# Kernel tuning notes

Measured on AMD Instinct MI355X. Metric: run time of the kernel, lower is better.

## Reference

```python
import jax, jax.numpy as jnp
import numpy as np

B, T, DIN, P, HID, L = 256, 512, 25, 128, 256, 5
Q = 0.15
EPS = 1e-5


def setup_inputs() -> dict:
    key = jax.random.key(0)
    ks = jax.random.split(key, 12)
    s = 0.05
    return {
        "x": jax.random.normal(ks[0], (B, T, DIN), jnp.float32),
        "lengths": jax.random.randint(ks[1], (B,), 1, T + 1),
        "ln_g": jnp.ones((DIN,), jnp.float32),
        "ln_b": jnp.zeros((DIN,), jnp.float32),
        "w1": jax.random.normal(ks[2], (DIN, P), jnp.float32) * s,
        "b1": jnp.zeros((P,), jnp.float32),
        "w2": jax.random.normal(ks[3], (P, P), jnp.float32) * s,
        "b2": jnp.zeros((P,), jnp.float32),
        "Wih0": jax.random.normal(ks[4], (2, 3 * HID, P), jnp.float32) * s,
        "Whh0": jax.random.normal(ks[5], (2, 3 * HID, HID), jnp.float32) * s,
        "bih0": jnp.zeros((2, 3 * HID), jnp.float32),
        "bhh0": jnp.zeros((2, 3 * HID), jnp.float32),
        "Wih": jax.random.normal(ks[6], (L - 1, 2, 3 * HID, 2 * HID), jnp.float32) * s,
        "Whh": jax.random.normal(ks[7], (L - 1, 2, 3 * HID, HID), jnp.float32) * s,
        "bih": jnp.zeros((L - 1, 2, 3 * HID), jnp.float32),
        "bhh": jnp.zeros((L - 1, 2, 3 * HID), jnp.float32),
        "Wc": jax.random.normal(ks[8], (2 * HID,), jnp.float32) * s,
        "bc": jnp.zeros((), jnp.float32),
    }


def _gru_dir(xs, mask, Wih, Whh, bih, bhh):
    """Masked unidirectional GRU (PyTorch gate convention). xs:[B,T,Din], mask:[B,T] -> [B,T,HID]."""
    xw = jnp.einsum('btd,gd->btg', xs, Wih) + bih  # [B,T,3H] precomputed input gates

    def step(h, inp):
        xw_t, m_t = inp  # [B,3H], [B]
        gh = h @ Whh.T + bhh
        r = jax.nn.sigmoid(xw_t[:, :HID] + gh[:, :HID])
        z = jax.nn.sigmoid(xw_t[:, HID:2 * HID] + gh[:, HID:2 * HID])
        n = jnp.tanh(xw_t[:, 2 * HID:] + r * gh[:, 2 * HID:])
        h_new = (1.0 - z) * n + z * h
        h = jnp.where(m_t[:, None], h_new, h)        # hold state past sequence end (packing)
        return h, jnp.where(m_t[:, None], h, 0.0)    # padded outputs are zero (pad_packed)

    h0 = jnp.zeros((xs.shape[0], HID), xs.dtype)
    _, ys = jax.lax.scan(step, h0, (xw.transpose(1, 0, 2), mask.T))
    return ys.transpose(1, 0, 2)


def reference(x, lengths, ln_g, ln_b, w1, b1, w2, b2,
              Wih0, Whh0, bih0, bhh0, Wih, Whh, bih, bhh, Wc, bc):
    mask = jnp.arange(T)[None, :] < lengths[:, None]  # [B,T]

    # InputProjection: LayerNorm -> Linear -> GELU(exact) -> Linear
    mu = x.mean(-1, keepdims=True)
    var = ((x - mu) ** 2).mean(-1, keepdims=True)
    xn = (x - mu) / jnp.sqrt(var + EPS) * ln_g + ln_b
    h = jax.nn.gelu(xn @ w1 + b1, approximate=False) @ w2 + b2  # [B,T,P]

    # per-sample time reversal indices (reverse valid prefix only)
    rev = jnp.clip(lengths[:, None] - 1 - jnp.arange(T)[None, :], 0, T - 1)  # [B,T]

    inp = h
    for l in range(L):
        Wi = Wih0 if l == 0 else Wih[l - 1]
        Wh = Whh0 if l == 0 else Whh[l - 1]
        bi = bih0 if l == 0 else bih[l - 1]
        bh = bhh0 if l == 0 else bhh[l - 1]
        yf = _gru_dir(inp, mask, Wi[0], Wh[0], bi[0], bh[0])
        x_rev = jnp.take_along_axis(inp, rev[:, :, None], axis=1) * mask[:, :, None]
        yb_rev = _gru_dir(x_rev, mask, Wi[1], Wh[1], bi[1], bh[1])
        yb = jnp.take_along_axis(yb_rev, rev[:, :, None], axis=1) * mask[:, :, None]
        inp = jnp.concatenate([yf, yb], axis=-1)  # [B,T,2H]
    H = inp

    # TopQPooling: per-sample variable-k top-k by L2-norm score, then mean
    scores = jnp.where(mask, jnp.linalg.norm(H, axis=2), -1e9)
    k_vals = jnp.maximum(jnp.ceil(lengths.astype(jnp.float32) * Q).astype(jnp.int32), 1)  # [B]
    order = jnp.argsort(-scores, axis=1)                      # descending by score
    topmask = jnp.arange(T)[None, :] < k_vals[:, None]        # first k of sorted order
    Hs = jnp.take_along_axis(H, order[:, :, None], axis=1)
    pooled = (Hs * topmask[:, :, None]).sum(axis=1) / k_vals[:, None].astype(H.dtype)

    logits = pooled @ Wc + bc  # [B]
    return logits
```

## Files before the change

### kernel.cpp

```cpp
#include <hip/hip_runtime.h>
#include <math.h>


#define CH 64

#define AT_LOAD_RLX(p)    __hip_atomic_load((p),  __ATOMIC_RELAXED, __HIP_MEMORY_SCOPE_AGENT)
#define AT_LOAD_ACQ(p)    __hip_atomic_load((p),  __ATOMIC_ACQUIRE, __HIP_MEMORY_SCOPE_AGENT)
#define AT_STORE_RLX(p,v) __hip_atomic_store((p),(v),__ATOMIC_RELAXED, __HIP_MEMORY_SCOPE_AGENT)
#define AT_STORE_REL(p,v) __hip_atomic_store((p),(v),__ATOMIC_RELEASE, __HIP_MEMORY_SCOPE_AGENT)

__global__ __launch_bounds__(256)
void sort_k(const int* __restrict__ len, int* __restrict__ perm,
            int* __restrict__ nchp, int Bg)
{
    __shared__ int ll[256];
    __shared__ int lp[256];
    const int i = threadIdx.x;
    const int li = len[i];
    ll[i] = li;
    __syncthreads();
    int rk = 0;
    for (int j = 0; j < 256; j++) {
        int lj = ll[j];
        rk += (lj < li || (lj == li && j < i)) ? 1 : 0;
    }
    lp[rk] = i;
    __syncthreads();
    perm[i] = lp[i];
    const int ngrp = 256 / Bg;
    if (i < ngrp) {
        int mx = ll[lp[i * Bg + Bg - 1]];
        int nch = (mx + 63) >> 6;
        nchp[i] = nch < 1 ? 1 : (nch > 8 ? 8 : nch);
    }
}

__global__ __launch_bounds__(256)
void prep_whhT_k(const float* __restrict__ Whh0, const float* __restrict__ Whh,
                 float* __restrict__ out)
{
    int id = blockIdx.x * 256 + threadIdx.x;
    int k  = id & 31;
    int q  = id >> 5;
    int g  = q % 3;  q /= 3;
    int t  = q & 255; q >>= 8;
    int sl = q & 7;   q >>= 3;
    int l  = q >> 1, d = q & 1;
    int row = g * 256 + sl * 32 + (t & 31);
    int col = (t >> 5) * 32 + k;
    out[id] = (l == 0) ? Whh0[(size_t)(d * 768 + row) * 256 + col]
                       : Whh[(size_t)(((l - 1) * 2 + d) * 768 + row) * 256 + col];
}

__global__ __launch_bounds__(128)
void input_proj_k(const float* __restrict__ x, const int* __restrict__ lengths,
                  const int* __restrict__ perm,
                  const float* __restrict__ lng, const float* __restrict__ lnb,
                  const float* __restrict__ w1, const float* __restrict__ b1v,
                  const float* __restrict__ w2, const float* __restrict__ b2v,
                  float* __restrict__ out, int g0)
{
    const int btl = blockIdx.x;
    const int sl  = btl >> 9;
    const int t   = btl & 511;
    const int b   = perm[g0 + sl];
    if (t >= lengths[b]) return;
    const int tid = threadIdx.x;
    __shared__ float xs[25];
    __shared__ float xn[25];
    __shared__ float hs[128];
    if (tid < 25) xs[tid] = x[((size_t)b * 512 + t) * 25 + tid];
    __syncthreads();
    if (tid < 25) {
        float mu = 0.f;
        #pragma unroll
        for (int k = 0; k < 25; k++) mu += xs[k];
        mu *= (1.f / 25.f);
        float var = 0.f;
        #pragma unroll
        for (int k = 0; k < 25; k++) { float dd = xs[k] - mu; var += dd * dd; }
        var *= (1.f / 25.f);
        float rstd = 1.f / sqrtf(var + 1e-5f);
        xn[tid] = (xs[tid] - mu) * rstd * lng[tid] + lnb[tid];
    }
    __syncthreads();
    float a = b1v[tid];
    #pragma unroll
    for (int k = 0; k < 25; k++) a = fmaf(xn[k], w1[k * 128 + tid], a);
    float ge = 0.5f * a * (1.f + erff(a * 0.70710678118654752440f));
    hs[tid] = ge;
    __syncthreads();
    float o = b2v[tid];
    #pragma unroll 8
    for (int k = 0; k < 128; k++) o = fmaf(hs[k], w2[k * 128 + tid], o);
    out[(size_t)btl * 128 + tid] = o;
}

__global__ __launch_bounds__(256, 1)
void round_k(const float* __restrict__ A, int K,
             const float* __restrict__ W,
             const float* __restrict__ bi,
             const int* __restrict__ lengths, const int* __restrict__ perm,
             const int* __restrict__ nchp, int gidx, int g0, int Bg,
             float* __restrict__ xw_w,
             const float* __restrict__ xw_r,
             const float* __restrict__ whhT,
             const float* __restrict__ bhh,
             float* __restrict__ Y,
             int* __restrict__ hx,
             int* __restrict__ flags,
             int NR, int r, int epoch)
{
    __shared__ float smem[8192];

    const int tid = threadIdx.x;
    const int nch = nchp[gidx];

    if ((int)blockIdx.x < NR) {
        if (r == 0) return;
        const int sgN = Bg >> 3;
        const int S2  = 2 * sgN;
        const int q   = (int)blockIdx.x % S2;
        const int sl  = (int)blockIdx.x / S2;
        const int d   = (q >= sgN) ? 1 : 0;
        const int sg  = q - d * sgN;
        const int lo  = d ? (nch - r) * CH : (r - 1) * CH;
        if (lo < 0 || lo >= 512) return;
        const int mlsg = lengths[perm[g0 + sg * 8 + 7]];
        int nst = min(lo + CH, mlsg) - lo;
        if (nst <= 0) return;
        const bool first = d ? (mlsg <= lo + CH) : (r == 1);

        float* hf   = smem;
        float* gsbp = smem + 2048;

        const int kq = tid >> 5;
        const int jj = tid & 31;

        const float* wb = whhT + ((size_t)(d * 8 + sl) * 256 + tid) * 96;
        float w0[32], w1[32], w2[32];
        #pragma unroll
        for (int k4 = 0; k4 < 8; k4++) {
            float4 a = *(const float4*)(wb + k4 * 4);
            float4 b = *(const float4*)(wb + 32 + k4 * 4);
            float4 c = *(const float4*)(wb + 64 + k4 * 4);
            w0[k4 * 4 + 0] = a.x; w0[k4 * 4 + 1] = a.y;
            w0[k4 * 4 + 2] = a.z; w0[k4 * 4 + 3] = a.w;
            w1[k4 * 4 + 0] = b.x; w1[k4 * 4 + 1] = b.y;
            w1[k4 * 4 + 2] = b.z; w1[k4 * 4 + 3] = b.w;
            w2[k4 * 4 + 0] = c.x; w2[k4 * 4 + 1] = c.y;
            w2[k4 * 4 + 2] = c.z; w2[k4 * 4 + 3] = c.w;
        }
        #pragma unroll
        for (int k = 0; k < 32; k++)
            asm volatile("" : "+v"(w0[k]), "+v"(w1[k]), "+v"(w2[k]));

        const int s2 = tid >> 5;
        const int j2 = tid & 31;
        const int lens2 = lengths[perm[g0 + sg * 8 + s2]];
        const float bh0 = bhh[d * 768 +       sl * 32 + j2];
        const float bh1 = bhh[d * 768 + 256 + sl * 32 + j2];
        const float bh2 = bhh[d * 768 + 512 + sl * 32 + j2];
        int* flg = flags + (size_t)((d * sgN + sg) * 8) * 64;
        const int PS  = 2 * Bg * 256;
        const int hxq = (d * Bg + sg * 8) * 256;

        if (first) {
            #pragma unroll
            for (int i = 0; i < 8; i++) hf[i * 256 + tid] = 0.f;
        } else {
            const int pprev = d ? (lo + nst) : (lo - 1);
            const int par0  = pprev & 1;
            const int* src = hx + par0 * PS + hxq;
            #pragma unroll
            for (int i = 0; i < 8; i++)
                hf[i * 256 + tid] = __int_as_float(AT_LOAD_RLX(src + i * 256 + tid));
        }
        __syncthreads();

        const float* xwd = xw_r + (size_t)(d * Bg + sg * 8) * 64 * 768 + sl * 32 + j2;

        for (int st = 0; st < nst; st++) {
            const int p   = d ? (lo + nst - 1 - st) : (lo + st);
            const int row = p - lo;
            const float* xr = xwd + (size_t)(s2 * 64 + row) * 768;
            const float xv0 = xr[0], xv1 = xr[256], xv2 = xr[512];

            #pragma unroll
            for (int s = 0; s < 8; s++) {
                float b0 = 0.f, b1 = 0.f, b2 = 0.f;
                #pragma unroll
                for (int k4 = 0; k4 < 8; k4++) {
                    const float4 h4 = *(const float4*)&hf[s * 256 + kq * 32 + k4 * 4];
                    b0 = fmaf(h4.x, w0[k4 * 4 + 0], b0);
                    b0 = fmaf(h4.y, w0[k4 * 4 + 1], b0);
                    b0 = fmaf(h4.z, w0[k4 * 4 + 2], b0);
                    b0 = fmaf(h4.w, w0[k4 * 4 + 3], b0);
                    b1 = fmaf(h4.x, w1[k4 * 4 + 0], b1);
                    b1 = fmaf(h4.y, w1[k4 * 4 + 1], b1);
                    b1 = fmaf(h4.z, w1[k4 * 4 + 2], b1);
                    b1 = fmaf(h4.w, w1[k4 * 4 + 3], b1);
                    b2 = fmaf(h4.x, w2[k4 * 4 + 0], b2);
                    b2 = fmaf(h4.y, w2[k4 * 4 + 1], b2);
                    b2 = fmaf(h4.z, w2[k4 * 4 + 2], b2);
                    b2 = fmaf(h4.w, w2[k4 * 4 + 3], b2);
                }
                gsbp[(kq * 8 + s) * 96 + jj]      = b0;
                gsbp[(kq * 8 + s) * 96 + 32 + jj] = b1;
                gsbp[(kq * 8 + s) * 96 + 64 + jj] = b2;
            }
            __syncthreads();

            float gr = bh0, gz = bh1, gn = bh2;
            #pragma unroll
            for (int qq = 0; qq < 8; qq++) {
                gr += gsbp[(qq * 8 + s2) * 96 + j2];
                gz += gsbp[(qq * 8 + s2) * 96 + 32 + j2];
                gn += gsbp[(qq * 8 + s2) * 96 + 64 + j2];
            }
            const float rg = 1.f / (1.f + expf(-(xv0 + gr)));
            const float zg = 1.f / (1.f + expf(-(xv1 + gz)));
            const float ng = tanhf(xv2 + rg * gn);
            const float hv = hf[s2 * 256 + sl * 32 + j2];
            float hn = (1.f - zg) * ng + zg * hv;
            if (p >= lens2) hn = hv;
            const int par = p & 1;
            AT_STORE_RLX(&hx[par * PS + hxq + s2 * 256 + sl * 32 + j2],
                         __float_as_int(hn));
            if (p < lens2)
                Y[((size_t)((sg * 8 + s2) * 512 + p)) * 512 + d * 256 + sl * 32 + j2] = hn;
            __syncthreads();

            if (st == nst - 1) break;
            if (tid == 0) AT_STORE_REL(&flg[sl * 64 + st], epoch);
            if (tid < 8) {
                int* f = &flg[tid * 64 + st];
                while (AT_LOAD_ACQ(f) != epoch) __builtin_amdgcn_s_sleep(2);
            }
            __syncthreads();
            {
                const int* src = hx + par * PS + hxq;
                #pragma unroll
                for (int i = 0; i < 8; i++)
                    hf[i * 256 + tid] = __int_as_float(
                        AT_LOAD_RLX(src + i * 256 + tid));
            }
            __syncthreads();
        }
    } else {
        float (*As)[68]  = (float(*)[68])smem;
        float (*Bs)[132] = (float(*)[132])(smem + 544);

        const int gid  = blockIdx.x - NR;
        const int nt   = gid % 6;
        const int rest = gid / 6;
        const int d    = (rest >= Bg) ? 1 : 0;
        const int s    = rest - d * Bg;
        const int lo   = d ? (nch - 1 - r) * 64 : r * 64;
        if (lo < 0 || lo >= 512) return;
        if (lengths[perm[g0 + s]] <= lo) return;

        float acc[4][8] = {};
        const int tm = tid >> 4;
        const int tn = tid & 15;
        const int arr = tid >> 2, ak = (tid & 3) * 2;
        const int bn = tid >> 1, bk = (tid & 1) * 4;

        const float* Ap = A + (size_t)(s * 512 + lo + arr) * K + ak;
        const float* Wp = W + ((size_t)d * 768 + nt * 128 + bn) * K + bk;

        for (int k0 = 0; k0 < K; k0 += 8) {
            float2 av = *(const float2*)(Ap + k0);
            float4 bv = *(const float4*)(Wp + k0);
            __syncthreads();
            As[ak][arr] = av.x; As[ak + 1][arr] = av.y;
            Bs[bk + 0][bn] = bv.x; Bs[bk + 1][bn] = bv.y;
            Bs[bk + 2][bn] = bv.z; Bs[bk + 3][bn] = bv.w;
            __syncthreads();
            #pragma unroll
            for (int kk = 0; kk < 8; kk++) {
                float4 a4 = *(const float4*)&As[kk][tm * 4];
                float4 b0v = *(const float4*)&Bs[kk][tn * 4];
                float4 b1v = *(const float4*)&Bs[kk][64 + tn * 4];
                float ar4[4] = {a4.x, a4.y, a4.z, a4.w};
                float br[8] = {b0v.x, b0v.y, b0v.z, b0v.w,
                               b1v.x, b1v.y, b1v.z, b1v.w};
                #pragma unroll
                for (int i = 0; i < 4; i++)
                    #pragma unroll
                    for (int j = 0; j < 8; j++)
                        acc[i][j] = fmaf(ar4[i], br[j], acc[i][j]);
            }
        }
        const int cb = d * 768 + nt * 128;
        float bv0[4], bv1[4];
        #pragma unroll
        for (int j = 0; j < 4; j++) {
            bv0[j] = bi[cb + tn * 4 + j];
            bv1[j] = bi[cb + 64 + tn * 4 + j];
        }
        #pragma unroll
        for (int i = 0; i < 4; i++) {
            const int row = tm * 4 + i;
            float* o = xw_w + (size_t)((d * Bg + s) * 64 + row) * 768 + nt * 128 + tn * 4;
            float4 c0 = make_float4(acc[i][0] + bv0[0], acc[i][1] + bv0[1],
                                    acc[i][2] + bv0[2], acc[i][3] + bv0[3]);
            float4 c1 = make_float4(acc[i][4] + bv1[0], acc[i][5] + bv1[1],
                                    acc[i][6] + bv1[2], acc[i][7] + bv1[3]);
            *(float4*)(o)      = c0;
            *(float4*)(o + 64) = c1;
        }
    }
}

__global__ __launch_bounds__(256)
void pool_k(const float* __restrict__ H, const int* __restrict__ lengths,
            const int* __restrict__ perm,
            const float* __restrict__ Wc, const float* __restrict__ bcp,
            float* __restrict__ out, int g0)
{
    const int bl = blockIdx.x;
    const int b  = perm[g0 + bl];
    const int tid = threadIdx.x;
    __shared__ float sc[512];
    __shared__ int   sel[128];
    __shared__ int   nsel;
    __shared__ float red[256];
    const int len = lengths[b];
    const int k = max(1, (int)ceilf((float)len * 0.15f));
    if (tid == 0) nsel = 0;
    for (int t = tid; t < 512; t += 256) {
        float s;
        if (t < len) {
            const float* row = H + ((size_t)bl * 512 + t) * 512;
            float acc = 0.f;
            for (int j = 0; j < 512; j++) acc = fmaf(row[j], row[j], acc);
            s = sqrtf(acc);
        } else s = -1e9f;
        sc[t] = s;
    }
    __syncthreads();
    for (int t = tid; t < 512; t += 256) {
        if (t < len) {
            const float s = sc[t];
            int cnt = 0;
            for (int u = 0; u < 512; u++) {
                float su = sc[u];
                cnt += (su > s || (su == s && u < t)) ? 1 : 0;
            }
            if (cnt < k) { int p = atomicAdd(&nsel, 1); sel[p] = t; }
        }
    }
    __syncthreads();
    const int ns = nsel;
    float part = 0.f;
    for (int j = tid; j < 512; j += 256) {
        float acc = 0.f;
        for (int i = 0; i < ns; i++)
            acc += H[((size_t)bl * 512 + sel[i]) * 512 + j];
        part += (acc / (float)k) * Wc[j];
    }
    red[tid] = part;
    __syncthreads();
    for (int s2 = 128; s2 > 0; s2 >>= 1) {
        if (tid < s2) red[tid] += red[tid + s2];
        __syncthreads();
    }
    if (tid == 0) out[b] = red[0] + bcp[0];
}

static inline size_t alup(size_t x) { return (x + 255) & ~255ull; }

static size_t tier_bytes(int Bg)
{
    return 2 * alup((size_t)Bg * 512 * 512 * 4)
         + 2 * alup((size_t)Bg * 2 * 64 * 768 * 4)
         + alup(1966080ull * 4)
         + alup((size_t)4 * Bg * 256 * 4)
         + alup((size_t)2 * (Bg / 8) * 8 * 64 * 4)
         + alup(2048);
}

extern "C" void kernel_launch(void* const* d_in, const int* in_sizes, int n_in,
                              void* d_out, int out_size, void* d_ws, size_t ws_size,
                              hipStream_t stream)
{
    const float* x    = (const float*)d_in[0];
    const int*   len  = (const int*)  d_in[1];
    const float* ln_g = (const float*)d_in[2];
    const float* ln_b = (const float*)d_in[3];
    const float* w1   = (const float*)d_in[4];
    const float* b1   = (const float*)d_in[5];
    const float* w2   = (const float*)d_in[6];
    const float* b2   = (const float*)d_in[7];
    const float* Wih0 = (const float*)d_in[8];
    const float* Whh0 = (const float*)d_in[9];
    const float* bih0 = (const float*)d_in[10];
    const float* bhh0 = (const float*)d_in[11];
    const float* Wih  = (const float*)d_in[12];
    const float* Whh  = (const float*)d_in[13];
    const float* bih  = (const float*)d_in[14];
    const float* bhh  = (const float*)d_in[15];
    const float* Wc   = (const float*)d_in[16];
    const float* bc   = (const float*)d_in[17];
    float* out = (float*)d_out;

    int Bg = 0;
    const int tiers[5] = {128, 64, 32, 16, 8};
    for (int i = 0; i < 5; i++)
        if (ws_size >= tier_bytes(tiers[i])) { Bg = tiers[i]; break; }
    if (Bg == 0) return;

    char* ws = (char*)d_ws;
    size_t off = 0;
    auto alloc = [&](size_t bytes) { size_t o = off; off += alup(bytes); return o; };
    float* h0    = (float*)(ws + alloc((size_t)Bg * 512 * 512 * 4));
    float* h1    = (float*)(ws + alloc((size_t)Bg * 512 * 512 * 4));
    float* xwA   = (float*)(ws + alloc((size_t)Bg * 2 * 64 * 768 * 4));
    float* xwB   = (float*)(ws + alloc((size_t)Bg * 2 * 64 * 768 * 4));
    float* whhT  = (float*)(ws + alloc(1966080ull * 4));
    int*   hx    = (int*)  (ws + alloc((size_t)4 * Bg * 256 * 4));
    const size_t flagBytes = (size_t)2 * (Bg / 8) * 8 * 64 * 4;
    int*   flags = (int*)  (ws + alloc(flagBytes));
    int*   perm  = (int*)  (ws + alloc(2048));
    int*   nchp  = perm + 256;
    float* xwbuf[2] = {xwA, xwB};

    hipMemsetAsync(flags, 0, flagBytes, stream);

    sort_k<<<1, 256, 0, stream>>>(len, perm, nchp, Bg);
    prep_whhT_k<<<7680, 256, 0, stream>>>(Whh0, Whh, whhT);

    const int NR = 2 * Bg;
    const int NG = 12 * Bg;

    for (int g0 = 0; g0 < 256; g0 += Bg) {
        const int gidx = g0 / Bg;
        input_proj_k<<<Bg * 512, 128, 0, stream>>>(x, len, perm, ln_g, ln_b,
                                                   w1, b1, w2, b2, h0, g0);
        float* bin = h0;
        float* bout = h1;
        for (int l = 0; l < 5; l++) {
            const int K = (l == 0) ? 128 : 512;
            const float* Wl  = (l == 0) ? Wih0 : (Wih + (size_t)(l - 1) * 2 * 768 * 512);
            const float* bil = (l == 0) ? bih0 : (bih + (size_t)(l - 1) * 1536);
            const float* whl = whhT + (size_t)l * 393216;
            const float* bhl = (l == 0) ? bhh0 : (bhh + (size_t)(l - 1) * 1536);
            for (int r = 0; r <= 8; r++) {
                const int ep = (gidx * 5 + l) * 9 + r + 1;
                round_k<<<NR + NG, 256, 0, stream>>>(
                    bin, K, Wl, bil, len, perm, nchp, gidx, g0, Bg,
                    xwbuf[r & 1], xwbuf[(r & 1) ^ 1],
                    whl, bhl, bout, hx, flags, NR, r, ep);
            }
            float* tmp = bin; bin = bout; bout = tmp;
        }
        pool_k<<<Bg, 256, 0, stream>>>(bin, len, perm, Wc, bc, out, g0);
    }
}
```

Measured before the change: 56.23 ms.

## Split fused round kernel into separate GEMM and recurrence launches, weights in LDS

Replaces the single launch that mixed input-projection GEMM blocks with recurrence blocks by two separate launches per round: gemm_k, then recur_k. The recurrence kernel now stages its recurrent weight slice in swizzled LDS instead of holding 96 floats per thread in registers, which frees VGPRs. In exchange the GEMM for the next chunk no longer overlaps with the current recurrence, there are more kernel launches, and each step adds LDS reads for the weights.

```diff
diff --git a/kernel.cpp b/kernel.cpp
--- a/kernel.cpp
+++ b/kernel.cpp
@@ -97,219 +97,220 @@
 }
 
 __global__ __launch_bounds__(256, 1)
-void round_k(const float* __restrict__ A, int K,
-             const float* __restrict__ W,
-             const float* __restrict__ bi,
-             const int* __restrict__ lengths, const int* __restrict__ perm,
+void recur_k(const int* __restrict__ lengths, const int* __restrict__ perm,
              const int* __restrict__ nchp, int gidx, int g0, int Bg,
-             float* __restrict__ xw_w,
              const float* __restrict__ xw_r,
              const float* __restrict__ whhT,
              const float* __restrict__ bhh,
              float* __restrict__ Y,
              int* __restrict__ hx,
              int* __restrict__ flags,
-             int NR, int r, int epoch)
-{
-    __shared__ float smem[8192];
+             int r, int epoch)
+{
+    __shared__ float wlds[24576];
+    __shared__ float hf[2048];
+    __shared__ float gsbp[6144];
 
     const int tid = threadIdx.x;
     const int nch = nchp[gidx];
-
-    if ((int)blockIdx.x < NR) {
-        if (r == 0) return;
-        const int sgN = Bg >> 3;
-        const int S2  = 2 * sgN;
-        const int q   = (int)blockIdx.x % S2;
-        const int sl  = (int)blockIdx.x / S2;
-        const int d   = (q >= sgN) ? 1 : 0;
-        const int sg  = q - d * sgN;
-        const int lo  = d ? (nch - r) * CH : (r - 1) * CH;
-        if (lo < 0 || lo >= 512) return;
-        const int mlsg = lengths[perm[g0 + sg * 8 + 7]];
-        int nst = min(lo + CH, mlsg) - lo;
-        if (nst <= 0) return;
-        const bool first = d ? (mlsg <= lo + CH) : (r == 1);
-
-        float* hf   = smem;
-        float* gsbp = smem + 2048;
-
-        const int kq = tid >> 5;
-        const int jj = tid & 31;
-
-        const float* wb = whhT + ((size_t)(d * 8 + sl) * 256 + tid) * 96;
-        float w0[32], w1[32], w2[32];
+    const int sgN = Bg >> 3;
+    const int S2  = 2 * sgN;
+    const int q   = (int)blockIdx.x % S2;
+    const int sl  = (int)blockIdx.x / S2;
+    const int d   = (q >= sgN) ? 1 : 0;
+    const int sg  = q - d * sgN;
+    const int lo  = d ? (nch - r) * CH : (r - 1) * CH;
+    if (lo < 0 || lo >= 512) return;
+    const int mlsg = lengths[perm[g0 + sg * 8 + 7]];
+    int nst = min(lo + CH, mlsg) - lo;
+    if (nst <= 0) return;
+    const bool first = d ? (mlsg <= lo + CH) : (r == 1);
+
+    const float* wb = whhT + ((size_t)(d * 8 + sl) * 256 + tid) * 96;
+    float* wt = wlds + tid * 96;
+    const int cx = tid & 7;
+    #pragma unroll
+    for (int i = 0; i < 24; i++) {
+        const float4 v = *(const float4*)(wb + i * 4);
+        *(float4*)(wt + ((i ^ cx) << 2)) = v;
+    }
+
+    const int kq = tid >> 5;
+    const int jj = tid & 31;
+    const int s2 = tid >> 5;
+    const int j2 = tid & 31;
+    const int lens2 = lengths[perm[g0 + sg * 8 + s2]];
+    const float bh0 = bhh[d * 768 +       sl * 32 + j2];
+    const float bh1 = bhh[d * 768 + 256 + sl * 32 + j2];
+    const float bh2 = bhh[d * 768 + 512 + sl * 32 + j2];
+    int* flg = flags + (size_t)((d * sgN + sg) * 8) * 64;
+    const int PS  = 2 * Bg * 256;
+    const int hxq = (d * Bg + sg * 8) * 256;
+
+    if (first) {
+        #pragma unroll
+        for (int i = 0; i < 8; i++) hf[i * 256 + tid] = 0.f;
+    } else {
+        const int pprev = d ? (lo + nst) : (lo - 1);
+        const int par0  = pprev & 1;
+        const int* src = hx + par0 * PS + hxq;
+        #pragma unroll
+        for (int i = 0; i < 8; i++)
+            hf[i * 256 + tid] = __int_as_float(AT_LOAD_RLX(src + i * 256 + tid));
+    }
+    __syncthreads();
+
+    const float* xwd = xw_r + (size_t)(d * Bg + sg * 8) * 64 * 768 + sl * 32 + j2;
+
+    for (int st = 0; st < nst; st++) {
+        const int p   = d ? (lo + nst - 1 - st) : (lo + st);
+        const int row = p - lo;
+        const float* xr = xwd + (size_t)(s2 * 64 + row) * 768;
+        const float xv0 = xr[0], xv1 = xr[256], xv2 = xr[512];
+
+        float a0[8], a1[8], a2[8];
+        #pragma unroll
+        for (int s = 0; s < 8; s++) { a0[s] = 0.f; a1[s] = 0.f; a2[s] = 0.f; }
         #pragma unroll
         for (int k4 = 0; k4 < 8; k4++) {
-            float4 a = *(const float4*)(wb + k4 * 4);
-            float4 b = *(const float4*)(wb + 32 + k4 * 4);
-            float4 c = *(const float4*)(wb + 64 + k4 * 4);
-            w0[k4 * 4 + 0] = a.x; w0[k4 * 4 + 1] = a.y;
-            w0[k4 * 4 + 2] = a.z; w0[k4 * 4 + 3] = a.w;
-            w1[k4 * 4 + 0] = b.x; w1[k4 * 4 + 1] = b.y;
-            w1[k4 * 4 + 2] = b.z; w1[k4 * 4 + 3] = b.w;
-            w2[k4 * 4 + 0] = c.x; w2[k4 * 4 + 1] = c.y;
-            w2[k4 * 4 + 2] = c.z; w2[k4 * 4 + 3] = c.w;
-        }
-        #pragma unroll
-        for (int k = 0; k < 32; k++)
-            asm volatile("" : "+v"(w0[k]), "+v"(w1[k]), "+v"(w2[k]));
-
-        const int s2 = tid >> 5;
-        const int j2 = tid & 31;
-        const int lens2 = lengths[perm[g0 + sg * 8 + s2]];
-        const float bh0 = bhh[d * 768 +       sl * 32 + j2];
-        const float bh1 = bhh[d * 768 + 256 + sl * 32 + j2];
-        const float bh2 = bhh[d * 768 + 512 + sl * 32 + j2];
-        int* flg = flags + (size_t)((d * sgN + sg) * 8) * 64;
-        const int PS  = 2 * Bg * 256;
-        const int hxq = (d * Bg + sg * 8) * 256;
-
-        if (first) {
+            const int sw = (k4 ^ cx) << 2;
+            const float4 w0 = *(const float4*)(wt + sw);
+            const float4 w1 = *(const float4*)(wt + 32 + sw);
+            const float4 w2 = *(const float4*)(wt + 64 + sw);
             #pragma unroll
-            for (int i = 0; i < 8; i++) hf[i * 256 + tid] = 0.f;
-        } else {
-            const int pprev = d ? (lo + nst) : (lo - 1);
-            const int par0  = pprev & 1;
-            const int* src = hx + par0 * PS + hxq;
+            for (int s = 0; s < 8; s++) {
+                const float4 h4 = *(const float4*)&hf[s * 256 + kq * 32 + k4 * 4];
+                a0[s] = fmaf(h4.x, w0.x, a0[s]);
+                a0[s] = fmaf(h4.y, w0.y, a0[s]);
+                a0[s] = fmaf(h4.z, w0.z, a0[s]);
+                a0[s] = fmaf(h4.w, w0.w, a0[s]);
+                a1[s] = fmaf(h4.x, w1.x, a1[s]);
+                a1[s] = fmaf(h4.y, w1.y, a1[s]);
+                a1[s] = fmaf(h4.z, w1.z, a1[s]);
+                a1[s] = fmaf(h4.w, w1.w, a1[s]);
+                a2[s] = fmaf(h4.x, w2.x, a2[s]);
+                a2[s] = fmaf(h4.y, w2.y, a2[s]);
+                a2[s] = fmaf(h4.z, w2.z, a2[s]);
+                a2[s] = fmaf(h4.w, w2.w, a2[s]);
+            }
+        }
+        #pragma unroll
+        for (int s = 0; s < 8; s++) {
+            gsbp[(kq * 8 + s) * 96 + jj]      = a0[s];
+            gsbp[(kq * 8 + s) * 96 + 32 + jj] = a1[s];
+            gsbp[(kq * 8 + s) * 96 + 64 + jj] = a2[s];
+        }
+        __syncthreads();
+
+        float gr = bh0, gz = bh1, gn = bh2;
+        #pragma unroll
+        for (int qq = 0; qq < 8; qq++) {
+            gr += gsbp[(qq * 8 + s2) * 96 + j2];
+            gz += gsbp[(qq * 8 + s2) * 96 + 32 + j2];
+            gn += gsbp[(qq * 8 + s2) * 96 + 64 + j2];
+        }
+        const float rg = 1.f / (1.f + expf(-(xv0 + gr)));
+        const float zg = 1.f / (1.f + expf(-(xv1 + gz)));
+        const float ng = tanhf(xv2 + rg * gn);
+        const float hv = hf[s2 * 256 + sl * 32 + j2];
+        float hn = (1.f - zg) * ng + zg * hv;
+        if (p >= lens2) hn = hv;
+        const int par = p & 1;
+        AT_STORE_RLX(&hx[par * PS + hxq + s2 * 256 + sl * 32 + j2],
+                     __float_as_int(hn));
+        if (p < lens2)
+            Y[((size_t)((sg * 8 + s2) * 512 + p)) * 512 + d * 256 + sl * 32 + j2] = hn;
+        __syncthreads();
+
+        if (st == nst - 1) break;
+        if (tid == 0) AT_STORE_REL(&flg[sl * 64 + st], epoch);
+        if (tid < 8) {
+            int* f = &flg[tid * 64 + st];
+            while (AT_LOAD_ACQ(f) != epoch) __builtin_amdgcn_s_sleep(2);
+        }
+        __syncthreads();
+        {
+            const int* src = hx + par * PS + hxq;
             #pragma unroll
             for (int i = 0; i < 8; i++)
-                hf[i * 256 + tid] = __int_as_float(AT_LOAD_RLX(src + i * 256 + tid));
-        }
-        __syncthreads();
-
-        const float* xwd = xw_r + (size_t)(d * Bg + sg * 8) * 64 * 768 + sl * 32 + j2;
-
-        for (int st = 0; st < nst; st++) {
-            const int p   = d ? (lo + nst - 1 - st) : (lo + st);
-            const int row = p - lo;
-            const float* xr = xwd + (size_t)(s2 * 64 + row) * 768;
-            const float xv0 = xr[0], xv1 = xr[256], xv2 = xr[512];
-
+                hf[i * 256 + tid] = __int_as_float(
+                    AT_LOAD_RLX(src + i * 256 + tid));
+        }
+        __syncthreads();
+    }
+}
+
+__global__ __launch_bounds__(256)
+void gemm_k(const float* __restrict__ A, int K,
+            const float* __restrict__ W,
+            const float* __restrict__ bi,
+            const int* __restrict__ lengths, const int* __restrict__ perm,
+            const int* __restrict__ nchp, int gidx, int g0, int Bg,
+            float* __restrict__ xw_w, int r)
+{
+    __shared__ float As[8][68];
+    __shared__ float Bs[8][132];
+
+    const int tid = threadIdx.x;
+    const int nch = nchp[gidx];
+    const int gid  = blockIdx.x;
+    const int nt   = gid % 6;
+    const int rest = gid / 6;
+    const int d    = (rest >= Bg) ? 1 : 0;
+    const int s    = rest - d * Bg;
+    const int lo   = d ? (nch - 1 - r) * 64 : r * 64;
+    if (lo < 0 || lo >= 512) return;
+    if (lengths[perm[g0 + s]] <= lo) return;
+
+    float acc[4][8] = {};
+    const int tm = tid >> 4;
+    const int tn = tid & 15;
+    const int arr = tid >> 2, ak = (tid & 3) * 2;
+    const int bn = tid >> 1, bk = (tid & 1) * 4;
+
+    const float* Ap = A + (size_t)(s * 512 + lo + arr) * K + ak;
+    const float* Wp = W + ((size_t)d * 768 + nt * 128 + bn) * K + bk;
+
+    for (int k0 = 0; k0 < K; k0 += 8) {
+        float2 av = *(const float2*)(Ap + k0);
+        float4 bv = *(const float4*)(Wp + k0);
+        __syncthreads();
+        As[ak][arr] = av.x; As[ak + 1][arr] = av.y;
+        Bs[bk + 0][bn] = bv.x; Bs[bk + 1][bn] = bv.y;
+        Bs[bk + 2][bn] = bv.z; Bs[bk + 3][bn] = bv.w;
+        __syncthreads();
+        #pragma unroll
+        for (int kk = 0; kk < 8; kk++) {
+            float4 a4 = *(const float4*)&As[kk][tm * 4];
+            float4 b0v = *(const float4*)&Bs[kk][tn * 4];
+            float4 b1v = *(const float4*)&Bs[kk][64 + tn * 4];
+            float ar4[4] = {a4.x, a4.y, a4.z, a4.w};
+            float br[8] = {b0v.x, b0v.y, b0v.z, b0v.w,
+                           b1v.x, b1v.y, b1v.z, b1v.w};
             #pragma unroll
-            for (int s = 0; s < 8; s++) {
-                float b0 = 0.f, b1 = 0.f, b2 = 0.f;
+            for (int i = 0; i < 4; i++)
                 #pragma unroll
-                for (int k4 = 0; k4 < 8; k4++) {
-                    const float4 h4 = *(const float4*)&hf[s * 256 + kq * 32 + k4 * 4];
-                    b0 = fmaf(h4.x, w0[k4 * 4 + 0], b0);
-                    b0 = fmaf(h4.y, w0[k4 * 4 + 1], b0);
-                    b0 = fmaf(h4.z, w0[k4 * 4 + 2], b0);
-                    b0 = fmaf(h4.w, w0[k4 * 4 + 3], b0);
-                    b1 = fmaf(h4.x, w1[k4 * 4 + 0], b1);
-                    b1 = fmaf(h4.y, w1[k4 * 4 + 1], b1);
-                    b1 = fmaf(h4.z, w1[k4 * 4 + 2], b1);
-                    b1 = fmaf(h4.w, w1[k4 * 4 + 3], b1);
-                    b2 = fmaf(h4.x, w2[k4 * 4 + 0], b2);
-                    b2 = fmaf(h4.y, w2[k4 * 4 + 1], b2);
-                    b2 = fmaf(h4.z, w2[k4 * 4 + 2], b2);
-                    b2 = fmaf(h4.w, w2[k4 * 4 + 3], b2);
-                }
-                gsbp[(kq * 8 + s) * 96 + jj]      = b0;
-                gsbp[(kq * 8 + s) * 96 + 32 + jj] = b1;
-                gsbp[(kq * 8 + s) * 96 + 64 + jj] = b2;
-            }
-            __syncthreads();
-
-            float gr = bh0, gz = bh1, gn = bh2;
-            #pragma unroll
-            for (int qq = 0; qq < 8; qq++) {
-                gr += gsbp[(qq * 8 + s2) * 96 + j2];
-                gz += gsbp[(qq * 8 + s2) * 96 + 32 + j2];
-                gn += gsbp[(qq * 8 + s2) * 96 + 64 + j2];
-            }
-            const float rg = 1.f / (1.f + expf(-(xv0 + gr)));
-            const float zg = 1.f / (1.f + expf(-(xv1 + gz)));
-            const float ng = tanhf(xv2 + rg * gn);
-            const float hv = hf[s2 * 256 + sl * 32 + j2];
-            float hn = (1.f - zg) * ng + zg * hv;
-            if (p >= lens2) hn = hv;
-            const int par = p & 1;
-            AT_STORE_RLX(&hx[par * PS + hxq + s2 * 256 + sl * 32 + j2],
-                         __float_as_int(hn));
-            if (p < lens2)
-                Y[((size_t)((sg * 8 + s2) * 512 + p)) * 512 + d * 256 + sl * 32 + j2] = hn;
-            __syncthreads();
-
-            if (st == nst - 1) break;
-            if (tid == 0) AT_STORE_REL(&flg[sl * 64 + st], epoch);
-            if (tid < 8) {
-                int* f = &flg[tid * 64 + st];
-                while (AT_LOAD_ACQ(f) != epoch) __builtin_amdgcn_s_sleep(2);
-            }
-            __syncthreads();
-            {
-                const int* src = hx + par * PS + hxq;
-                #pragma unroll
-                for (int i = 0; i < 8; i++)
-                    hf[i * 256 + tid] = __int_as_float(
-                        AT_LOAD_RLX(src + i * 256 + tid));
-            }
-            __syncthreads();
-        }
-    } else {
-        float (*As)[68]  = (float(*)[68])smem;
-        float (*Bs)[132] = (float(*)[132])(smem + 544);
-
-        const int gid  = blockIdx.x - NR;
-        const int nt   = gid % 6;
-        const int rest = gid / 6;
-        const int d    = (rest >= Bg) ? 1 : 0;
-        const int s    = rest - d * Bg;
-        const int lo   = d ? (nch - 1 - r) * 64 : r * 64;
-        if (lo < 0 || lo >= 512) return;
-        if (lengths[perm[g0 + s]] <= lo) return;
-
-        float acc[4][8] = {};
-        const int tm = tid >> 4;
-        const int tn = tid & 15;
-        const int arr = tid >> 2, ak = (tid & 3) * 2;
-        const int bn = tid >> 1, bk = (tid & 1) * 4;
-
-        const float* Ap = A + (size_t)(s * 512 + lo + arr) * K + ak;
-        const float* Wp = W + ((size_t)d * 768 + nt * 128 + bn) * K + bk;
-
-        for (int k0 = 0; k0 < K; k0 += 8) {
-            float2 av = *(const float2*)(Ap + k0);
-            float4 bv = *(const float4*)(Wp + k0);
-            __syncthreads();
-            As[ak][arr] = av.x; As[ak + 1][arr] = av.y;
-            Bs[bk + 0][bn] = bv.x; Bs[bk + 1][bn] = bv.y;
-            Bs[bk + 2][bn] = bv.z; Bs[bk + 3][bn] = bv.w;
-            __syncthreads();
-            #pragma unroll
-            for (int kk = 0; kk < 8; kk++) {
-                float4 a4 = *(const float4*)&As[kk][tm * 4];
-                float4 b0v = *(const float4*)&Bs[kk][tn * 4];
-                float4 b1v = *(const float4*)&Bs[kk][64 + tn * 4];
-                float ar4[4] = {a4.x, a4.y, a4.z, a4.w};
-                float br[8] = {b0v.x, b0v.y, b0v.z, b0v.w,
-                               b1v.x, b1v.y, b1v.z, b1v.w};
-                #pragma unroll
-                for (int i = 0; i < 4; i++)
-                    #pragma unroll
-                    for (int j = 0; j < 8; j++)
-                        acc[i][j] = fmaf(ar4[i], br[j], acc[i][j]);
-            }
-        }
-        const int cb = d * 768 + nt * 128;
-        float bv0[4], bv1[4];
-        #pragma unroll
-        for (int j = 0; j < 4; j++) {
-            bv0[j] = bi[cb + tn * 4 + j];
-            bv1[j] = bi[cb + 64 + tn * 4 + j];
-        }
-        #pragma unroll
-        for (int i = 0; i < 4; i++) {
-            const int row = tm * 4 + i;
-            float* o = xw_w + (size_t)((d * Bg + s) * 64 + row) * 768 + nt * 128 + tn * 4;
-            float4 c0 = make_float4(acc[i][0] + bv0[0], acc[i][1] + bv0[1],
-                                    acc[i][2] + bv0[2], acc[i][3] + bv0[3]);
-            float4 c1 = make_float4(acc[i][4] + bv1[0], acc[i][5] + bv1[1],
-                                    acc[i][6] + bv1[2], acc[i][7] + bv1[3]);
-            *(float4*)(o)      = c0;
-            *(float4*)(o + 64) = c1;
-        }
+                for (int j = 0; j < 8; j++)
+                    acc[i][j] = fmaf(ar4[i], br[j], acc[i][j]);
+        }
+    }
+    const int cb = d * 768 + nt * 128;
+    float bv0[4], bv1[4];
+    #pragma unroll
+    for (int j = 0; j < 4; j++) {
+        bv0[j] = bi[cb + tn * 4 + j];
+        bv1[j] = bi[cb + 64 + tn * 4 + j];
+    }
+    #pragma unroll
+    for (int i = 0; i < 4; i++) {
+        const int row = tm * 4 + i;
+        float* o = xw_w + (size_t)((d * Bg + s) * 64 + row) * 768 + nt * 128 + tn * 4;
+        float4 c0 = make_float4(acc[i][0] + bv0[0], acc[i][1] + bv0[1],
+                                acc[i][2] + bv0[2], acc[i][3] + bv0[3]);
+        float4 c1 = make_float4(acc[i][4] + bv1[0], acc[i][5] + bv1[1],
+                                acc[i][6] + bv1[2], acc[i][7] + bv1[3]);
+        *(float4*)(o)      = c0;
+        *(float4*)(o + 64) = c1;
     }
 }
 
@@ -447,11 +448,17 @@
             const float* whl = whhT + (size_t)l * 393216;
             const float* bhl = (l == 0) ? bhh0 : (bhh + (size_t)(l - 1) * 1536);
             for (int r = 0; r <= 8; r++) {
-                const int ep = (gidx * 5 + l) * 9 + r + 1;
-                round_k<<<NR + NG, 256, 0, stream>>>(
-                    bin, K, Wl, bil, len, perm, nchp, gidx, g0, Bg,
-                    xwbuf[r & 1], xwbuf[(r & 1) ^ 1],
-                    whl, bhl, bout, hx, flags, NR, r, ep);
+                if (r < 8)
+                    gemm_k<<<NG, 256, 0, stream>>>(bin, K, Wl, bil, len, perm,
+                                                   nchp, gidx, g0, Bg,
+                                                   xwbuf[r & 1], r);
+                if (r >= 1) {
+                    const int ep = (gidx * 5 + l) * 9 + r + 1;
+                    recur_k<<<NR, 256, 0, stream>>>(len, perm, nchp, gidx, g0, Bg,
+                                                    xwbuf[(r & 1) ^ 1],
+                                                    whl, bhl, bout, hx, flags,
+                                                    r, ep);
+                }
             }
             float* tmp = bin; bin = bout; bout = tmp;
         }
```

Result: slower. 63.26 ms (+12.5%).
